# Optimization experiments

Measured on AMD Instinct MI355X. Metric: run time of the kernel, lower is better.

The kernel has to match this reference:

```python
import jax, jax.numpy as jnp
import numpy as np

EPS = 1e-08
K_N = 10
K_E = 10
F_DIM = 512
SCALE = F_DIM ** -0.5
N_NODES = 16384
N_EDGES = 2048


def layernorm(x, w, b):
    mu = x.mean(axis=-1, keepdims=True)
    var = x.var(axis=-1, keepdims=True)
    return (x - mu) * jax.lax.rsqrt(var + 1e-5) * w + b


def mask_attn(attn, k):
    # topk along last dim, scatter boolean mask, elementwise masking
    _, idx = jax.lax.top_k(attn, k)
    rows = jnp.arange(attn.shape[0])[:, None]
    mask = jnp.zeros(attn.shape, dtype=bool).at[rows, idx].set(True)
    return attn * mask


def setup_inputs() -> dict:
    key = jax.random.key(0)
    ks = jax.random.split(key, 12)
    d, h = F_DIM, 512  # hidden = max(f_dim, 128)
    w = 0.02  # weight init scale to keep softmax unsaturated
    return {
        'inputs': jax.random.normal(ks[0], (N_NODES, d), jnp.float32),
        'noise': jax.random.normal(ks[1], (N_EDGES, d), jnp.float32),
        'edges_mu': jax.random.normal(ks[2], (1, d), jnp.float32),
        'edges_logsigma': jnp.zeros((1, d), jnp.float32),
        'Wq': jax.random.normal(ks[3], (d, d), jnp.float32) * w,
        'bq': jnp.zeros((d,), jnp.float32),
        'Wk': jax.random.normal(ks[4], (d, d), jnp.float32) * w,
        'bk': jnp.zeros((d,), jnp.float32),
        'Wv': jax.random.normal(ks[5], (d, d), jnp.float32) * w,
        'bv': jnp.zeros((d,), jnp.float32),
        'W1': jax.random.normal(ks[6], (2 * d, h), jnp.float32) * w,
        'b1': jnp.zeros((h,), jnp.float32),
        'W2': jax.random.normal(ks[7], (h, d), jnp.float32) * w,
        'b2': jnp.zeros((d,), jnp.float32),
        'ln_in_w': jnp.ones((d,), jnp.float32),
        'ln_in_b': jnp.zeros((d,), jnp.float32),
        'ln_e_w': jnp.ones((d,), jnp.float32),
        'ln_e_b': jnp.zeros((d,), jnp.float32),
    }


def reference(inputs, noise, edges_mu, edges_logsigma, Wq, bq, Wk, bk, Wv, bv,
              W1, b1, W2, b2, ln_in_w, ln_in_b, ln_e_w, ln_e_b):
    relu = jax.nn.relu
    # slot init: mu + sigma * noise  -> [n_s, d]
    edges = edges_mu + jnp.exp(edges_logsigma) * noise
    x = layernorm(inputs, ln_in_w, ln_in_b)          # [n, d]
    k = relu(x @ Wk + bk)                            # [n, d]
    v = relu(x @ Wv + bv)                            # [n, d]
    # single iteration (iters=1)
    e = layernorm(edges, ln_e_w, ln_e_b)             # [n_s, d]
    q = relu(e @ Wq + bq)                            # [n_s, d]
    dots = (q @ k.T) * SCALE                         # [n_s, n]
    attn = jax.nn.softmax(dots, axis=1) + EPS
    attn = attn / attn.sum(axis=1, keepdims=True)
    attn = mask_attn(attn, K_N)
    updates = attn @ v                               # [n_s, d]
    e = jnp.concatenate([e, updates], axis=1)        # [n_s, 2d]
    e = relu(e @ W1 + b1) @ W2 + b2                  # mlp -> [n_s, d]
    q2 = x @ Wq + bq                                 # note: no activation here
    k2 = relu(e @ Wk + bk)                           # [n_s, d]
    dots2 = (q2 @ k2.T) * SCALE                      # [n, n_s]
    attn_v = jax.nn.softmax(dots2, axis=1)
    H = mask_attn(attn_v, K_E)
    return e, H, dots2
```

## Files before the change

### kernel.cpp

```cpp
#include <hip/hip_runtime.h>
#include <stdint.h>


#define NN 16384
#define NE 2048
#define TOPK 10

static const float SCALE_F = 0.04419417382415922f;
#define EPS_F 1e-8f

using bf16x8  = __attribute__((ext_vector_type(8))) __bf16;
using floatx4 = __attribute__((ext_vector_type(4))) float;

__device__ __forceinline__ unsigned f_as_u(float f) {
  union { float f; unsigned u; } v; v.f = f; return v.u;
}
__device__ __forceinline__ float u_as_f(unsigned u) {
  union { unsigned u; float f; } v; v.u = u; return v.f;
}
__device__ __forceinline__ unsigned short f2bf(float f) {
  unsigned u = f_as_u(f);
  unsigned r = u + 0x7fffu + ((u >> 16) & 1u);
  return (unsigned short)(r >> 16);
}
__device__ __forceinline__ float bf2f(unsigned short h) {
  return u_as_f(((unsigned)h) << 16);
}

__device__ __forceinline__ void glds16(const unsigned short* g, unsigned short* l) {
  __builtin_amdgcn_global_load_lds(
      (const __attribute__((address_space(1))) unsigned int*)g,
      (__attribute__((address_space(3))) unsigned int*)l, 16, 0, 0);
}

__device__ __forceinline__ unsigned fkey(float f) {
  unsigned u = f_as_u(f);
  return (u & 0x80000000u) ? ~u : (u | 0x80000000u);
}
__device__ __forceinline__ float funkey(unsigned k) {
  unsigned u = (k & 0x80000000u) ? (k ^ 0x80000000u) : ~k;
  return u_as_f(u);
}
__device__ __forceinline__ unsigned long long packkc(float v, int col) {
  return ((unsigned long long)fkey(v) << 32) | (unsigned)(~(unsigned)col);
}
__device__ __forceinline__ int unpack_col(unsigned long long w) {
  return (int)(~(unsigned)(w & 0xFFFFFFFFull));
}
__device__ __forceinline__ float unpack_val(unsigned long long w) {
  return funkey((unsigned)(w >> 32));
}
__device__ __forceinline__ unsigned long long shfl_xor_u64(unsigned long long x, int m) {
  unsigned lo = (unsigned)x, hi = (unsigned)(x >> 32);
  lo = __shfl_xor(lo, m, 64);
  hi = __shfl_xor(hi, m, 64);
  return ((unsigned long long)hi << 32) | lo;
}

__global__ void transpose_all_kernel(
    const float* __restrict__ Wk, const float* __restrict__ Wv,
    const float* __restrict__ Wq, unsigned short* __restrict__ WcatT,
    const float* __restrict__ W1, unsigned short* __restrict__ W1Th,
    unsigned short* __restrict__ W1Tl,
    const float* __restrict__ W2, unsigned short* __restrict__ W2Th,
    unsigned short* __restrict__ W2Tl) {
  __shared__ float tile[32][33];
  int z = blockIdx.z;
  if (z != 3 && blockIdx.y >= 16) return;
  const float* src;
  unsigned short* dhi;
  unsigned short* dlo;
  int K;
  if (z < 3) {
    src = z == 0 ? Wk : (z == 1 ? Wv : Wq);
    dhi = WcatT + (size_t)z * 512 * 512;
    dlo = nullptr; K = 512;
  } else if (z == 3) {
    src = W1; dhi = W1Th; dlo = W1Tl; K = 1024;
  } else {
    src = W2; dhi = W2Th; dlo = W2Tl; K = 512;
  }
  int n0 = blockIdx.x * 32, k0 = blockIdx.y * 32;
  int tx = threadIdx.x, ty = threadIdx.y;
  for (int r = ty; r < 32; r += 8)
    tile[r][tx] = src[(size_t)(k0 + r) * 512 + n0 + tx];
  __syncthreads();
  for (int r = ty; r < 32; r += 8) {
    float v = tile[tx][r];
    size_t o = (size_t)(n0 + r) * K + k0 + tx;
    unsigned short h = f2bf(v);
    dhi[o] = h;
    if (dlo) dlo[o] = f2bf(v - bf2f(h));
  }
}

__device__ __forceinline__ float block_sum_256(float v, float* sm4) {
#pragma unroll
  for (int off = 32; off; off >>= 1) v += __shfl_down(v, off, 64);
  __syncthreads();
  if ((threadIdx.x & 63) == 0) sm4[threadIdx.x >> 6] = v;
  __syncthreads();
  return (sm4[0] + sm4[1]) + (sm4[2] + sm4[3]);
}

__global__ __launch_bounds__(256) void ln_all_kernel(
    const float* __restrict__ in, const float* __restrict__ w,
    const float* __restrict__ b, unsigned short* __restrict__ out_hi,
    const float* __restrict__ noise, const float* __restrict__ mu_e,
    const float* __restrict__ ls_e, const float* __restrict__ we,
    const float* __restrict__ be, unsigned short* __restrict__ e1_hi,
    unsigned short* __restrict__ e1_lo) {
  __shared__ float sm4[4];
  int row = blockIdx.x, tid = threadIdx.x;
  if (row < NN) {
    const float* r = in + (size_t)row * 512;
    float x0 = r[tid], x1 = r[tid + 256];
    float mu = block_sum_256(x0 + x1, sm4) * (1.0f / 512.0f);
    float d0 = x0 - mu, d1 = x1 - mu;
    float var = block_sum_256(d0 * d0 + d1 * d1, sm4) * (1.0f / 512.0f);
    float rs = rsqrtf(var + 1e-5f);
    out_hi[(size_t)row * 512 + tid]       = f2bf(d0 * rs * w[tid] + b[tid]);
    out_hi[(size_t)row * 512 + tid + 256] = f2bf(d1 * rs * w[tid + 256] + b[tid + 256]);
  } else {
    row -= NN;
    const float* r = noise + (size_t)row * 512;
    float x0 = mu_e[tid] + expf(ls_e[tid]) * r[tid];
    float x1 = mu_e[tid + 256] + expf(ls_e[tid + 256]) * r[tid + 256];
    float mu = block_sum_256(x0 + x1, sm4) * (1.0f / 512.0f);
    float d0 = x0 - mu, d1 = x1 - mu;
    float var = block_sum_256(d0 * d0 + d1 * d1, sm4) * (1.0f / 512.0f);
    float rs = rsqrtf(var + 1e-5f);
    float y0 = d0 * rs * we[tid] + be[tid];
    float y1 = d1 * rs * we[tid + 256] + be[tid + 256];
    size_t o = (size_t)row * 1024;
    unsigned short h0 = f2bf(y0), h1 = f2bf(y1);
    e1_hi[o + tid] = h0;             e1_lo[o + tid] = f2bf(y0 - bf2f(h0));
    e1_hi[o + tid + 256] = h1;       e1_lo[o + tid + 256] = f2bf(y1 - bf2f(h1));
  }
}

#define GEMM128_CORE(A_, LDA_, B_, bm_, bn_, acc_, SMEM_)                      \
  unsigned short* As = (unsigned short*)(SMEM_);                               \
  unsigned short* Bs = (unsigned short*)(SMEM_) + 8192;                        \
  {                                                                            \
    int srow = tid >> 3;                                                       \
    int scol = ((tid ^ (tid >> 3)) & 7) << 3;                                  \
    const unsigned short* gA = (A_) + ((bm_) + srow) * (size_t)(LDA_) + scol;  \
    const unsigned short* gB = (B_) + ((bn_) + srow) * (size_t)512 + scol;     \
    unsigned short* dA = As + wave * 512;                                      \
    unsigned short* dB = Bs + wave * 512;                                      \
    int swz0 = (quad ^ (lrow & 7)) << 3;                                       \
    int swz1 = swz0 ^ 32;                                                      \
    int aoff0 = (wave * 32 + lrow) * 64;                                       \
    int aoff1 = aoff0 + 16 * 64;                                               \
    int boffl = lrow * 64;                                                     \
    for (int k0 = 0; k0 < 512; k0 += 64) {                                     \
      glds16(gA + k0, dA);                                                     \
      glds16(gA + 32 * (size_t)(LDA_) + k0, dA + 2048);                        \
      glds16(gA + 64 * (size_t)(LDA_) + k0, dA + 4096);                        \
      glds16(gA + 96 * (size_t)(LDA_) + k0, dA + 6144);                        \
      glds16(gB + k0, dB);                                                     \
      glds16(gB + 32 * 512 + k0, dB + 2048);                                   \
      glds16(gB + 64 * 512 + k0, dB + 4096);                                   \
      glds16(gB + 96 * 512 + k0, dB + 6144);                                   \
      __syncthreads();                                                         \
      bf16x8 af00 = *(const bf16x8*)&As[aoff0 + swz0];                         \
      bf16x8 af01 = *(const bf16x8*)&As[aoff0 + swz1];                         \
      bf16x8 af10 = *(const bf16x8*)&As[aoff1 + swz0];                         \
      bf16x8 af11 = *(const bf16x8*)&As[aoff1 + swz1];                         \
      _Pragma("unroll")                                                        \
      for (int t = 0; t < 8; ++t) {                                            \
        bf16x8 bf0 = *(const bf16x8*)&Bs[t * 1024 + boffl + swz0];             \
        bf16x8 bf1 = *(const bf16x8*)&Bs[t * 1024 + boffl + swz1];             \
        acc_[0][t] = __builtin_amdgcn_mfma_f32_16x16x32_bf16(af00, bf0, acc_[0][t], 0, 0, 0); \
        acc_[0][t] = __builtin_amdgcn_mfma_f32_16x16x32_bf16(af01, bf1, acc_[0][t], 0, 0, 0); \
        acc_[1][t] = __builtin_amdgcn_mfma_f32_16x16x32_bf16(af10, bf0, acc_[1][t], 0, 0, 0); \
        acc_[1][t] = __builtin_amdgcn_mfma_f32_16x16x32_bf16(af11, bf1, acc_[1][t], 0, 0, 0); \
      }                                                                        \
      __syncthreads();                                                         \
    }                                                                          \
  }

#define XCD_PANEL_MAP(mt_, nt_, owns_m_)                                       \
  int xcd = bid & 7, idx = bid >> 3;                                           \
  int per = ((owns_m_) ? (mt_) : (nt_)) >> 3;                                  \
  int pa = idx % per, pb = idx / per;                                          \
  bm = (size_t)((owns_m_) ? (xcd * per + pa) : pb) * 128;                      \
  bn = (size_t)((owns_m_) ? pb : (xcd * per + pa)) * 128;

__global__ __launch_bounds__(256) void gemm128_dots_kernel(
    const unsigned short* __restrict__ A, const unsigned short* __restrict__ B,
    float alpha, float* __restrict__ C, int ldc, int mt, int nt, int owns_m,
    float2* __restrict__ stats) {
  __shared__ __align__(16) char smem[33792];
  int tid = threadIdx.x, wave = tid >> 6, lane = tid & 63;
  int lrow = lane & 15, quad = lane >> 4;
  int bid = (int)blockIdx.x;
  size_t bm, bn;
  XCD_PANEL_MAP(mt, nt, owns_m)
  floatx4 zero4 = {0.f, 0.f, 0.f, 0.f};
  floatx4 acc[2][8];
#pragma unroll
  for (int i = 0; i < 2; ++i)
#pragma unroll
    for (int t = 0; t < 8; ++t) acc[i][t] = zero4;
  GEMM128_CORE(A, 512, B, bm, bn, acc, smem)
  __syncthreads();
  float* wb = (float*)smem + wave * (16 * 132);
#pragma unroll
  for (int i = 0; i < 2; ++i) {
#pragma unroll
    for (int t = 0; t < 8; ++t)
#pragma unroll
      for (int r = 0; r < 4; ++r)
        wb[(quad * 4 + r) * 132 + t * 16 + lrow] = acc[i][t][r] * alpha;
    __syncthreads();
    size_t rowbase = bm + wave * 32 + i * 16;
#pragma unroll
    for (int p = 0; p < 8; ++p) {
      int rr = p * 2 + (lane >> 5);
      float4 v = *(const float4*)&wb[rr * 132 + ((lane & 31) << 2)];
      *(float4*)&C[(rowbase + rr) * (size_t)ldc + bn + ((lane & 31) << 2)] = v;
    }
    __syncthreads();
  }
  if (stats) {
    int j = (int)(bn >> 7);
#pragma unroll
    for (int i = 0; i < 2; ++i) {
#pragma unroll
      for (int r = 0; r < 4; ++r) {
        float mv = acc[i][0][r];
#pragma unroll
        for (int t = 1; t < 8; ++t) mv = fmaxf(mv, acc[i][t][r]);
#pragma unroll
        for (int sft = 1; sft < 16; sft <<= 1)
          mv = fmaxf(mv, __shfl_xor(mv, sft, 64));
        float m = mv * alpha;
        float s = 0.f;
#pragma unroll
        for (int t = 0; t < 8; ++t)
          s += __expf(acc[i][t][r] * alpha - m);
#pragma unroll
        for (int sft = 1; sft < 16; sft <<= 1) s += __shfl_xor(s, sft, 64);
        if (lrow == 0) {
          int row = (int)bm + wave * 32 + i * 16 + quad * 4 + r;
          stats[(size_t)row * 128 + j] = make_float2(m, s);
        }
      }
    }
  }
}

__global__ __launch_bounds__(256) void gemm128_kvq_kernel(
    const unsigned short* __restrict__ X, const unsigned short* __restrict__ E1,
    const unsigned short* __restrict__ B,
    const float* __restrict__ bk, const float* __restrict__ bv,
    const float* __restrict__ bq,
    unsigned short* __restrict__ khi, unsigned short* __restrict__ vhi,
    unsigned short* __restrict__ q2hi, unsigned short* __restrict__ qhi) {
  __shared__ __align__(16) char smem[32768];
  int tid = threadIdx.x, wave = tid >> 6, lane = tid & 63;
  int lrow = lane & 15, quad = lane >> 4;
  int bid = (int)blockIdx.x;
  size_t bm, bn;
  const unsigned short* Aptr;
  int lda;
  unsigned short* dst;
  const float* bias;
  bool relu;
  if (bid < 1536) {
    XCD_PANEL_MAP(128, 12, 1)
    Aptr = X; lda = 512;
    int mat = (int)(bn >> 9);
    bias = mat == 0 ? bk : (mat == 1 ? bv : bq);
    dst = mat == 0 ? khi : (mat == 1 ? vhi : q2hi);
    relu = mat < 2;
  } else {
    int qb = bid - 1536;
    bm = (size_t)(qb >> 2) * 128;
    bn = 1024 + (size_t)(qb & 3) * 128;
    Aptr = E1; lda = 1024;
    dst = qhi; bias = bq; relu = true;
  }
  int colbase = (int)(bn & 511);
  floatx4 zero4 = {0.f, 0.f, 0.f, 0.f};
  floatx4 acc[2][8];
#pragma unroll
  for (int i = 0; i < 2; ++i)
#pragma unroll
    for (int t = 0; t < 8; ++t) acc[i][t] = zero4;
  GEMM128_CORE(Aptr, lda, B, bm, bn, acc, smem)
  __syncthreads();
  unsigned short* wb = (unsigned short*)smem + wave * (16 * 136);
#pragma unroll
  for (int i = 0; i < 2; ++i) {
#pragma unroll
    for (int t = 0; t < 8; ++t) {
      float bvv = bias[colbase + t * 16 + lrow];
#pragma unroll
      for (int r = 0; r < 4; ++r) {
        float v = acc[i][t][r] + bvv;
        if (relu) v = fmaxf(v, 0.0f);
        wb[(quad * 4 + r) * 136 + t * 16 + lrow] = f2bf(v);
      }
    }
    __syncthreads();
    size_t rowbase = bm + wave * 32 + i * 16;
#pragma unroll
    for (int p = 0; p < 4; ++p) {
      int rr = p * 4 + (lane >> 4);
      uint4 v = *(const uint4*)&wb[rr * 136 + ((lane & 15) << 3)];
      *(uint4*)&dst[(rowbase + rr) * 512 + colbase + ((lane & 15) << 3)] = v;
    }
    __syncthreads();
  }
}

template <bool SPLIT, bool RELU, bool HAS_BIAS, bool WF32, bool WHI, bool WLO>
__global__ __launch_bounds__(256) void gemm64_kernel(
    const unsigned short* __restrict__ Ahi, const unsigned short* __restrict__ Alo, int lda,
    const unsigned short* __restrict__ Bhi, const unsigned short* __restrict__ Blo, int K,
    const float* __restrict__ bias, float alpha,
    float* __restrict__ Cf, int ldc,
    unsigned short* __restrict__ Chi, unsigned short* __restrict__ Clo, int ldcb) {
  __shared__ __align__(16) unsigned short AsH[64 * 32];
  __shared__ __align__(16) unsigned short BsH[64 * 32];
  __shared__ __align__(16) unsigned short AsL[64 * 32];
  __shared__ __align__(16) unsigned short BsL[64 * 32];
  int tid = threadIdx.x, wave = tid >> 6, lane = tid & 63;
  int lrow = lane & 15, quad = lane >> 4;
  size_t bm = (size_t)blockIdx.x * 64, bn = (size_t)blockIdx.y * 64;
  int row = tid >> 2, off = (tid & 3) << 3;
  size_t aoff = (bm + row) * (size_t)lda + off;
  size_t boff = (bn + row) * (size_t)K + off;

  floatx4 zero4 = {0.f, 0.f, 0.f, 0.f};
  floatx4 acc[4];
#pragma unroll
  for (int t = 0; t < 4; ++t) acc[t] = zero4;

  uint4 ah = *(const uint4*)(Ahi + aoff);
  uint4 bh = *(const uint4*)(Bhi + boff);
  uint4 al, bl;
  if (SPLIT) {
    al = *(const uint4*)(Alo + aoff);
    bl = *(const uint4*)(Blo + boff);
  }
  for (int k0 = 0; k0 < K; k0 += 32) {
    __syncthreads();
    *(uint4*)&AsH[tid * 8] = ah;
    *(uint4*)&BsH[tid * 8] = bh;
    if (SPLIT) {
      *(uint4*)&AsL[tid * 8] = al;
      *(uint4*)&BsL[tid * 8] = bl;
    }
    __syncthreads();
    if (k0 + 32 < K) {
      ah = *(const uint4*)(Ahi + aoff + k0 + 32);
      bh = *(const uint4*)(Bhi + boff + k0 + 32);
      if (SPLIT) {
        al = *(const uint4*)(Alo + aoff + k0 + 32);
        bl = *(const uint4*)(Blo + boff + k0 + 32);
      }
    }
    int ai = (wave * 16 + lrow) * 32 + quad * 8;
    bf16x8 aH = *(const bf16x8*)&AsH[ai];
    bf16x8 aL;
    if (SPLIT) aL = *(const bf16x8*)&AsL[ai];
#pragma unroll
    for (int t = 0; t < 4; ++t) {
      int bi = (t * 16 + lrow) * 32 + quad * 8;
      bf16x8 bH = *(const bf16x8*)&BsH[bi];
      acc[t] = __builtin_amdgcn_mfma_f32_16x16x32_bf16(aH, bH, acc[t], 0, 0, 0);
      if (SPLIT) {
        bf16x8 bL = *(const bf16x8*)&BsL[bi];
        acc[t] = __builtin_amdgcn_mfma_f32_16x16x32_bf16(aH, bL, acc[t], 0, 0, 0);
        acc[t] = __builtin_amdgcn_mfma_f32_16x16x32_bf16(aL, bH, acc[t], 0, 0, 0);
      }
    }
  }
  size_t row0 = bm + wave * 16 + quad * 4;
#pragma unroll
  for (int t = 0; t < 4; ++t) {
    int col = (int)bn + t * 16 + lrow;
    float bv = HAS_BIAS ? bias[col] : 0.0f;
#pragma unroll
    for (int r = 0; r < 4; ++r) {
      float v = acc[t][r] * alpha + bv;
      if (RELU) v = fmaxf(v, 0.0f);
      if (WF32) Cf[(row0 + r) * (size_t)ldc + col] = v;
      if (WHI) {
        unsigned short h = f2bf(v);
        Chi[(row0 + r) * (size_t)ldcb + col] = h;
        if (WLO) Clo[(row0 + r) * (size_t)ldcb + col] = f2bf(v - bf2f(h));
      }
    }
  }
}

#define INSERT4(lv, li, v, col)                                   \
  do {                                                            \
    if ((v) > lv[3]) {                                            \
      float cv_ = (v); int ci_ = (col);                           \
      _Pragma("unroll")                                           \
      for (int j_ = 0; j_ < 4; ++j_) {                            \
        bool sw_ = (cv_ > lv[j_]);                                \
        float tv_ = sw_ ? lv[j_] : cv_;                           \
        int ti_ = sw_ ? li[j_] : ci_;                              \
        lv[j_] = sw_ ? cv_ : lv[j_];                              \
        li[j_] = sw_ ? ci_ : li[j_];                              \
        cv_ = tv_; ci_ = ti_;                                     \
      }                                                           \
    }                                                             \
  } while (0)

__global__ __launch_bounds__(256) void attn1_kernel(
    const float* __restrict__ dots,
    const float2* __restrict__ stats,
    const unsigned short* __restrict__ vhi,
    unsigned short* __restrict__ e1_hi, unsigned short* __restrict__ e1_lo) {
  __shared__ float sm_m[128], sm_s[128];
  __shared__ unsigned long long sm_key[128];
  __shared__ int clist[128], jpos[128];
  __shared__ int sh_c;
  __shared__ float sh_red[4];
  __shared__ float sh_M, sh_th;
  __shared__ unsigned long long wbest[4];
  __shared__ unsigned long long wkey_s[TOPK];

  int tid = threadIdx.x, wave = tid >> 6, lane = tid & 63;
  int rowi = blockIdx.x;
  const float* drow = dots + (size_t)rowi * NN;

  if (tid < 128) {
    float2 ms = stats[(size_t)rowi * 128 + tid];
    sm_m[tid] = ms.x; sm_s[tid] = ms.y;
    sm_key[tid] = packkc(ms.x, tid);
  }
  if (tid == 0) sh_c = 0;
  __syncthreads();

  if (tid < 128) {
    unsigned long long mykey = sm_key[tid];
    int cnt = 0;
    for (int i = 0; i < 128; ++i) cnt += (sm_key[i] > mykey) ? 1 : 0;
    if (cnt == 0) sh_M = sm_m[tid];
    if (cnt == 9) sh_th = sm_m[tid];
  }
  __syncthreads();
  float M = sh_M, th = sh_th;

  float zp = (tid < 128) ? sm_s[tid] * __expf(sm_m[tid] - M) : 0.f;
#pragma unroll
  for (int off = 32; off; off >>= 1) zp += __shfl_down(zp, off, 64);
  if (lane == 0) sh_red[wave] = zp;
  if (tid < 128 && sm_m[tid] >= th) {
    int p = atomicAdd(&sh_c, 1);
    clist[p] = tid;
    jpos[tid] = p;
  }
  __syncthreads();
  float Z = (sh_red[0] + sh_red[1]) + (sh_red[2] + sh_red[3]);
  int c = sh_c;
  int nel = c << 7;

  float lv[4]; int li[4];
#pragma unroll
  for (int j = 0; j < 4; ++j) { lv[j] = -INFINITY; li[j] = 0x7fffffff; }
  for (int idx = tid; idx < nel; idx += 256) {
    int jj = clist[idx >> 7];
    int col = (jj << 7) + (idx & 127);
    float v = drow[col];
    INSERT4(lv, li, v, col);
  }

  unsigned long long selmask = 0ull;
  int taken = 0;
  for (int rnd = 0; rnd < TOPK; ++rnd) {
    unsigned long long key;
    if (taken < 4) {
      key = packkc(lv[0], li[0]);
    } else {
      key = 0ull;
      int p = 0;
      for (int idx = tid; idx < nel; idx += 256, ++p) {
        if (!((selmask >> p) & 1ull)) {
          int jj = clist[idx >> 7];
          int col = (jj << 7) + (idx & 127);
          unsigned long long kk = packkc(drow[col], col);
          if (kk > key) key = kk;
        }
      }
    }
#pragma unroll
    for (int sft = 32; sft; sft >>= 1) {
      unsigned long long ok = shfl_xor_u64(key, sft);
      if (ok > key) key = ok;
    }
    if (lane == 0) wbest[wave] = key;
    __syncthreads();
    unsigned long long w = wbest[0];
    if (wbest[1] > w) w = wbest[1];
    if (wbest[2] > w) w = wbest[2];
    if (wbest[3] > w) w = wbest[3];
    if (tid == 0) wkey_s[rnd] = w;
    int wcol = unpack_col(w);
    int widx = (jpos[wcol >> 7] << 7) + (wcol & 127);
    if ((widx & 255) == tid) {
      selmask |= (1ull << (widx >> 8));
      if (taken < 4) {
#pragma unroll
        for (int j = 0; j < 3; ++j) { lv[j] = lv[j + 1]; li[j] = li[j + 1]; }
      }
      ++taken;
    }
    __syncthreads();
  }

  const float inv_den = 1.0f / (1.0f + (float)NN * EPS_F);
  float invZ = 1.0f / Z;
  float u0 = 0.f, u1 = 0.f;
#pragma unroll
  for (int j = 0; j < TOPK; ++j) {
    unsigned long long w = wkey_s[j];
    int col = unpack_col(w);
    float val = unpack_val(w);
    float a = (__expf(val - M) * invZ + EPS_F) * inv_den;
    const unsigned short* vr = vhi + (size_t)col * 512;
    u0 += a * bf2f(vr[tid]);
    u1 += a * bf2f(vr[tid + 256]);
  }
  size_t o = (size_t)rowi * 1024 + 512;
  unsigned short h0 = f2bf(u0), h1 = f2bf(u1);
  e1_hi[o + tid] = h0;             e1_lo[o + tid] = f2bf(u0 - bf2f(h0));
  e1_hi[o + tid + 256] = h1;       e1_lo[o + tid + 256] = f2bf(u1 - bf2f(h1));
}

__global__ __launch_bounds__(256) void attn2_kernel(const float* __restrict__ dots2,
                                                    float* __restrict__ Hout) {
  int tid = threadIdx.x, wave = tid >> 6, lane = tid & 63;
  int rowi = blockIdx.x * 4 + wave;
  const float4* r4 = (const float4*)(dots2 + (size_t)rowi * NE);

  float d[32];
  float m = -INFINITY;
#pragma unroll
  for (int i = 0; i < 8; ++i) {
    float4 q = r4[lane + (i << 6)];
#pragma unroll
    for (int c = 0; c < 4; ++c) {
      d[i * 4 + c] = (&q.x)[c];
      m = fmaxf(m, d[i * 4 + c]);
    }
  }
#pragma unroll
  for (int sft = 32; sft; sft >>= 1) m = fmaxf(m, __shfl_xor(m, sft, 64));

  float s = 0.f;
#pragma unroll
  for (int j = 0; j < 32; ++j) { d[j] = __expf(d[j] - m); s += d[j]; }
#pragma unroll
  for (int sft = 32; sft; sft >>= 1) s += __shfl_xor(s, sft, 64);
  float invZ = 1.0f / s;

  float lv[4]; int li[4];
#pragma unroll
  for (int j = 0; j < 4; ++j) { lv[j] = -INFINITY; li[j] = 0x7fffffff; }
#pragma unroll
  for (int i = 0; i < 8; ++i) {
#pragma unroll
    for (int c = 0; c < 4; ++c) {
      int col = ((lane + (i << 6)) << 2) + c;
      INSERT4(lv, li, d[i * 4 + c], col);
    }
  }

  unsigned selmask = 0;
  int taken = 0;
  for (int rnd = 0; rnd < TOPK; ++rnd) {
    unsigned long long key;
    if (taken < 4) {
      key = packkc(lv[0], li[0]);
    } else {
      key = 0ull;
#pragma unroll
      for (int j = 0; j < 32; ++j) {
        if (!((selmask >> j) & 1u)) {
          int col = ((lane + ((j >> 2) << 6)) << 2) + (j & 3);
          unsigned long long kk = packkc(d[j], col);
          if (kk > key) key = kk;
        }
      }
    }
#pragma unroll
    for (int sft = 32; sft; sft >>= 1) {
      unsigned long long ok = shfl_xor_u64(key, sft);
      if (ok > key) key = ok;
    }
    int wcol = unpack_col(key);
    if (((wcol >> 2) & 63) == lane) {
      int sl = ((wcol >> 8) << 2) | (wcol & 3);
      selmask |= (1u << sl);
      if (taken < 4) {
#pragma unroll
        for (int j = 0; j < 3; ++j) { lv[j] = lv[j + 1]; li[j] = li[j + 1]; }
      }
      ++taken;
    }
  }

  float* hr = Hout + (size_t)rowi * NE;
#pragma unroll
  for (int i = 0; i < 8; ++i) {
    float4 o;
#pragma unroll
    for (int c = 0; c < 4; ++c) {
      int sl = i * 4 + c;
      (&o.x)[c] = ((selmask >> sl) & 1u) ? d[sl] * invZ : 0.0f;
    }
    ((float4*)hr)[lane + (i << 6)] = o;
  }
}

extern "C" void kernel_launch(void* const* d_in, const int* in_sizes, int n_in,
                              void* d_out, int out_size, void* d_ws, size_t ws_size,
                              hipStream_t stream) {
  (void)in_sizes; (void)n_in; (void)out_size; (void)ws_size;
  const float* inputs  = (const float*)d_in[0];
  const float* noise   = (const float*)d_in[1];
  const float* edges_mu = (const float*)d_in[2];
  const float* edges_ls = (const float*)d_in[3];
  const float* Wq = (const float*)d_in[4];
  const float* bq = (const float*)d_in[5];
  const float* Wk = (const float*)d_in[6];
  const float* bk = (const float*)d_in[7];
  const float* Wv = (const float*)d_in[8];
  const float* bv = (const float*)d_in[9];
  const float* W1 = (const float*)d_in[10];
  const float* b1 = (const float*)d_in[11];
  const float* W2 = (const float*)d_in[12];
  const float* b2 = (const float*)d_in[13];
  const float* ln_in_w = (const float*)d_in[14];
  const float* ln_in_b = (const float*)d_in[15];
  const float* ln_e_w = (const float*)d_in[16];
  const float* ln_e_b = (const float*)d_in[17];

  float* out_e  = (float*)d_out;
  float* out_H  = out_e + (size_t)NE * 512;
  float* out_d2 = out_H + (size_t)NN * NE;

  const size_t MB = 1024 * 1024;
  unsigned char* hb = (unsigned char*)out_H;
  unsigned short* x_hi  = (unsigned short*)(hb);
  unsigned short* k_hi  = (unsigned short*)(hb + 16 * MB);
  unsigned short* v_hi  = (unsigned short*)(hb + 32 * MB);
  unsigned short* q2_hi = (unsigned short*)(hb + 48 * MB);
  unsigned short* WcatT = (unsigned short*)(hb + 64 * MB);
  unsigned short* W1Th  = (unsigned short*)(hb + 66 * MB);
  unsigned short* W1Tl  = (unsigned short*)(hb + 67 * MB);
  unsigned short* W2Th  = (unsigned short*)(hb + 68 * MB);
  unsigned short* W2Tl  = (unsigned short*)(hb + 68 * MB + 512 * 1024);
  unsigned short* e1_hi = (unsigned short*)(hb + 70 * MB);
  unsigned short* e1_lo = (unsigned short*)(hb + 74 * MB);
  unsigned short* q_hi  = (unsigned short*)(hb + 78 * MB);
  unsigned short* h_hi  = (unsigned short*)(hb + 80 * MB);
  unsigned short* h_lo  = (unsigned short*)(hb + 82 * MB);
  unsigned short* e_hi  = (unsigned short*)(hb + 84 * MB);
  float2* stats1        = (float2*)(hb + 86 * MB);
  unsigned short* WkT   = WcatT;
  float* dots = out_d2;
  unsigned short* k2_hi = (unsigned short*)d_ws;

  dim3 tb(256);
  dim3 t32(32, 8);

  transpose_all_kernel<<<dim3(16, 32, 5), t32, 0, stream>>>(
      Wk, Wv, Wq, WcatT, W1, W1Th, W1Tl, W2, W2Th, W2Tl);
  ln_all_kernel<<<NN + NE, tb, 0, stream>>>(
      inputs, ln_in_w, ln_in_b, x_hi,
      noise, edges_mu, edges_ls, ln_e_w, ln_e_b, e1_hi, e1_lo);

  gemm128_kvq_kernel<<<dim3(1600), tb, 0, stream>>>(
      x_hi, e1_hi, WcatT, bk, bv, bq, k_hi, v_hi, q2_hi, q_hi);
  gemm128_dots_kernel<<<dim3(2048), tb, 0, stream>>>(
      q_hi, k_hi, SCALE_F, dots, NN, 16, 128, 0, stats1);
  attn1_kernel<<<NE, tb, 0, stream>>>(dots, stats1, v_hi, e1_hi, e1_lo);
  gemm64_kernel<true, true, true, false, true, true><<<dim3(32, 8), tb, 0, stream>>>(
      e1_hi, e1_lo, 1024, W1Th, W1Tl, 1024, b1, 1.f, nullptr, 0, h_hi, h_lo, 512);
  gemm64_kernel<true, false, true, true, true, false><<<dim3(32, 8), tb, 0, stream>>>(
      h_hi, h_lo, 512, W2Th, W2Tl, 512, b2, 1.f, out_e, 512, e_hi, nullptr, 512);
  gemm64_kernel<false, true, true, false, true, false><<<dim3(32, 8), tb, 0, stream>>>(
      e_hi, nullptr, 512, WkT, nullptr, 512, bk, 1.f, nullptr, 0, k2_hi, nullptr, 512);
  gemm128_dots_kernel<<<dim3(2048), tb, 0, stream>>>(
      q2_hi, k2_hi, SCALE_F, out_d2, NE, 128, 16, 1, nullptr);
  attn2_kernel<<<NN / 4, tb, 0, stream>>>(out_d2, out_H);
}
```

Baseline: 551.6 us.

## Replace 128x128 dots GEMM with 256x256 tile, 8-wave pipelined MFMA kernel

Both dots GEMMs (q·kᵀ and q2·k2ᵀ) now use a 256x256 tile kernel with 512 threads. It stages tiles through a 128KB LDS ring via direct global-to-LDS loads, using explicit vmcnt waits, barriers and setprio around MFMA phases. The softmax row statistics move from register shuffles into the LDS epilogue. The larger tile is meant to raise arithmetic intensity and overlap loads with MFMA, at the cost of heavy LDS use, lower occupancy and a hand-scheduled pipeline that is fragile.

```diff
diff --git a/kernel.cpp b/kernel.cpp
--- a/kernel.cpp
+++ b/kernel.cpp
@@ -188,67 +188,162 @@
   bm = (size_t)((owns_m_) ? (xcd * per + pa) : pb) * 128;                      \
   bn = (size_t)((owns_m_) ? pb : (xcd * per + pa)) * 128;
 
-__global__ __launch_bounds__(256) void gemm128_dots_kernel(
+
+#define NOVM ((void)0)
+#define VM2 asm volatile("s_waitcnt vmcnt(2)" ::: "memory")
+#define VM0 asm volatile("s_waitcnt vmcnt(0)" ::: "memory")
+#define NOSTAGE ((void)0)
+
+#define STAGE(G_, rowbase_, kb_, slotptr_)                                     \
+  { const unsigned short* g0_ =                                                \
+        (G_) + ((rowbase_) + (size_t)sr0) * 512 + (kb_) + sc0;                 \
+    const unsigned short* g1_ =                                                \
+        (G_) + ((rowbase_) + (size_t)sr1) * 512 + (kb_) + sc1;                 \
+    glds16(g0_, (unsigned short*)((char*)(slotptr_) + wave * 1024));           \
+    glds16(g1_, (unsigned short*)((char*)(slotptr_) + 8192 + wave * 1024)); }
+
+#define PHASE(IM0_, IN0_, ASL_, BSL_, STAGE_STMT_, VM_)                        \
+  {                                                                            \
+    const char* Ap_ = ldsA_c + (ASL_) * 16384;                                 \
+    const char* Bp_ = ldsB_c + (BSL_) * 16384;                                 \
+    bf16x8 af_[4][2], bg_[2][2];                                               \
+    _Pragma("unroll") for (int i_ = 0; i_ < 4; ++i_) {                         \
+      af_[i_][0] = *(const bf16x8*)(Ap_ + aoff0 + i_ * 4096);                  \
+      af_[i_][1] = *(const bf16x8*)(Ap_ + aoff1 + i_ * 4096);                  \
+    }                                                                          \
+    _Pragma("unroll") for (int j_ = 0; j_ < 2; ++j_) {                         \
+      bg_[j_][0] = *(const bf16x8*)(Bp_ + boff0 + j_ * 8192);                  \
+      bg_[j_][1] = *(const bf16x8*)(Bp_ + boff1 + j_ * 8192);                  \
+    }                                                                          \
+    STAGE_STMT_;                                                               \
+    VM_;                                                                       \
+    __builtin_amdgcn_sched_barrier(0);                                         \
+    __builtin_amdgcn_s_barrier();                                              \
+    __builtin_amdgcn_sched_barrier(0);                                         \
+    __builtin_amdgcn_s_setprio(1);                                             \
+    _Pragma("unroll") for (int i_ = 0; i_ < 4; ++i_)                           \
+      _Pragma("unroll") for (int j_ = 0; j_ < 2; ++j_) {                       \
+        acc[(IM0_) + i_][(IN0_) + j_] =                                        \
+            __builtin_amdgcn_mfma_f32_16x16x32_bf16(                           \
+                af_[i_][0], bg_[j_][0], acc[(IM0_) + i_][(IN0_) + j_], 0, 0, 0);\
+        acc[(IM0_) + i_][(IN0_) + j_] =                                        \
+            __builtin_amdgcn_mfma_f32_16x16x32_bf16(                           \
+                af_[i_][1], bg_[j_][1], acc[(IM0_) + i_][(IN0_) + j_], 0, 0, 0);\
+      }                                                                        \
+    __builtin_amdgcn_s_setprio(0);                                             \
+  }
+
+#define GEMM256_CORE(A_, B_)                                                   \
+  __shared__ __align__(16) char lds_all[131072];                               \
+  char* ldsA_s = lds_all;                                                      \
+  char* ldsB_s = lds_all + 65536;                                              \
+  const char* ldsA_c = lds_all;                                                \
+  const char* ldsB_c = lds_all + 65536;                                        \
+  int tid = threadIdx.x, wave = tid >> 6, lane = tid & 63;                     \
+  int lrow = lane & 15, quad = lane >> 4;                                      \
+  int wfm = wave >> 2, wfn = wave & 3;                                         \
+  int smask = ((lrow >> 2) & 3) << 5;                                          \
+  int aoff0 = (wfm * 16 + lrow) * 128 + ((quad * 16) ^ smask);                 \
+  int aoff1 = aoff0 ^ 64;                                                      \
+  int boff0 = (wfn * 16 + lrow) * 128 + ((quad * 16) ^ smask);                 \
+  int boff1 = boff0 ^ 64;                                                      \
+  int p0_ = tid * 16, l0_ = p0_ ^ (((p0_ >> 9) & 3) << 5);                     \
+  int sr0 = l0_ >> 7, sc0 = (l0_ & 127) >> 1;                                  \
+  int p1_ = 8192 + tid * 16, l1_ = p1_ ^ (((p1_ >> 9) & 3) << 5);              \
+  int sr1 = l1_ >> 7, sc1 = (l1_ & 127) >> 1;                                  \
+  floatx4 acc[8][4];                                                           \
+  { floatx4 z4_ = {0.f, 0.f, 0.f, 0.f};                                        \
+    _Pragma("unroll") for (int i_ = 0; i_ < 8; ++i_)                           \
+      _Pragma("unroll") for (int j_ = 0; j_ < 4; ++j_) acc[i_][j_] = z4_; }    \
+        \
+  STAGE(A_, bm, 0, ldsA_s)                                                     \
+  STAGE(B_, bn, 0, ldsB_s)                                                     \
+  STAGE(A_, bm + 128, 0, ldsA_s + 16384)                                       \
+  STAGE(B_, bn + 128, 0, ldsB_s + 16384)                                       \
+  STAGE(A_, bm, 64, ldsA_s + 32768)                                            \
+  VM2;                                                                         \
+  __builtin_amdgcn_sched_barrier(0);                                           \
+  __builtin_amdgcn_s_barrier();                                                \
+  __builtin_amdgcn_sched_barrier(0);                                           \
+  for (int t2 = 0; t2 < 8; t2 += 2) {                                          \
+    int kn = (t2 + 1) * 64, kn2 = (t2 + 2) * 64, kn3 = (t2 + 3) * 64;          \
+    PHASE(0, 0, 0, 0, STAGE(B_, bn, kn, ldsB_s + 32768), NOVM)                 \
+    PHASE(0, 2, 0, 1, STAGE(A_, bm + 128, kn, ldsA_s + 49152), NOVM)           \
+    PHASE(4, 0, 1, 0, STAGE(B_, bn + 128, kn, ldsB_s + 49152), NOVM)           \
+    if (t2 < 6) {                                                              \
+      PHASE(4, 2, 1, 1, STAGE(A_, bm, kn2, ldsA_s), VM2)                       \
+      PHASE(0, 0, 2, 2, STAGE(B_, bn, kn2, ldsB_s), NOVM)                      \
+      PHASE(0, 2, 2, 3, STAGE(A_, bm + 128, kn2, ldsA_s + 16384), NOVM)        \
+      PHASE(4, 0, 3, 2, STAGE(B_, bn + 128, kn2, ldsB_s + 16384), NOVM)        \
+      PHASE(4, 2, 3, 3, STAGE(A_, bm, kn3, ldsA_s + 32768), VM2)               \
+    } else {                                                                   \
+      PHASE(4, 2, 1, 1, NOSTAGE, VM0)                                          \
+      PHASE(0, 0, 2, 2, NOSTAGE, NOVM)                                         \
+      PHASE(0, 2, 2, 3, NOSTAGE, NOVM)                                         \
+      PHASE(4, 0, 3, 2, NOSTAGE, NOVM)                                         \
+      PHASE(4, 2, 3, 3, NOSTAGE, NOVM)                                         \
+    }                                                                          \
+    (void)kn3;                                                                 \
+  }
+
+__global__ __launch_bounds__(512, 2) void gemm256_dots_kernel(
     const unsigned short* __restrict__ A, const unsigned short* __restrict__ B,
     float alpha, float* __restrict__ C, int ldc, int mt, int nt, int owns_m,
     float2* __restrict__ stats) {
-  __shared__ __align__(16) char smem[33792];
-  int tid = threadIdx.x, wave = tid >> 6, lane = tid & 63;
-  int lrow = lane & 15, quad = lane >> 4;
   int bid = (int)blockIdx.x;
   size_t bm, bn;
-  XCD_PANEL_MAP(mt, nt, owns_m)
-  floatx4 zero4 = {0.f, 0.f, 0.f, 0.f};
-  floatx4 acc[2][8];
-#pragma unroll
-  for (int i = 0; i < 2; ++i)
-#pragma unroll
-    for (int t = 0; t < 8; ++t) acc[i][t] = zero4;
-  GEMM128_CORE(A, 512, B, bm, bn, acc, smem)
+  {
+    int xcd = bid & 7, idx = bid >> 3;
+    int per = (owns_m ? mt : nt) >> 3;
+    int pa = idx % per, pb = idx / per;
+    bm = (size_t)(owns_m ? (xcd * per + pa) : pb) * 256;
+    bn = (size_t)(owns_m ? pb : (xcd * per + pa)) * 256;
+  }
+  GEMM256_CORE(A, B)
   __syncthreads();
-  float* wb = (float*)smem + wave * (16 * 132);
-#pragma unroll
-  for (int i = 0; i < 2; ++i) {
-#pragma unroll
-    for (int t = 0; t < 8; ++t)
-#pragma unroll
-      for (int r = 0; r < 4; ++r)
-        wb[(quad * 4 + r) * 132 + t * 16 + lrow] = acc[i][t][r] * alpha;
+  float* eb = (float*)lds_all;
+#pragma unroll
+  for (int g = 0; g < 4; ++g) {
+#pragma unroll
+    for (int imh = 0; imh < 2; ++imh) {
+      int im = 2 * g + imh;
+      int rloc = imh * 32 + wfm * 16 + quad * 4;
+#pragma unroll
+      for (int in = 0; in < 4; ++in) {
+        int cloc = in * 64 + wfn * 16 + lrow;
+#pragma unroll
+        for (int r = 0; r < 4; ++r)
+          eb[(rloc + r) * 260 + cloc] = acc[im][in][r] * alpha;
+      }
+    }
     __syncthreads();
-    size_t rowbase = bm + wave * 32 + i * 16;
+    size_t rowg = bm + 64 * g;
 #pragma unroll
     for (int p = 0; p < 8; ++p) {
-      int rr = p * 2 + (lane >> 5);
-      float4 v = *(const float4*)&wb[rr * 132 + ((lane & 31) << 2)];
-      *(float4*)&C[(rowbase + rr) * (size_t)ldc + bn + ((lane & 31) << 2)] = v;
+      int f = tid + (p << 9);
+      int rr = f >> 6, c4 = (f & 63) << 2;
+      float4 v = *(const float4*)&eb[rr * 260 + c4];
+      *(float4*)&C[(rowg + rr) * (size_t)ldc + bn + c4] = v;
+    }
+    if (stats) {
+      int task = tid >> 2, sub = tid & 3;
+      int rr = task >> 1, jt = task & 1;
+      const float* base = &eb[rr * 260 + jt * 128 + sub * 32];
+      float mv = base[0];
+#pragma unroll
+      for (int u = 1; u < 32; ++u) mv = fmaxf(mv, base[u]);
+#pragma unroll
+      for (int sft = 1; sft < 4; sft <<= 1)
+        mv = fmaxf(mv, __shfl_xor(mv, sft, 64));
+      float sl = 0.f;
+#pragma unroll
+      for (int u = 0; u < 32; ++u) sl += __expf(base[u] - mv);
+#pragma unroll
+      for (int sft = 1; sft < 4; sft <<= 1) sl += __shfl_xor(sl, sft, 64);
+      if (sub == 0)
+        stats[(rowg + rr) * 128 + (int)(bn >> 7) + jt] = make_float2(mv, sl);
     }
     __syncthreads();
-  }
-  if (stats) {
-    int j = (int)(bn >> 7);
-#pragma unroll
-    for (int i = 0; i < 2; ++i) {
-#pragma unroll
-      for (int r = 0; r < 4; ++r) {
-        float mv = acc[i][0][r];
-#pragma unroll
-        for (int t = 1; t < 8; ++t) mv = fmaxf(mv, acc[i][t][r]);
-#pragma unroll
-        for (int sft = 1; sft < 16; sft <<= 1)
-          mv = fmaxf(mv, __shfl_xor(mv, sft, 64));
-        float m = mv * alpha;
-        float s = 0.f;
-#pragma unroll
-        for (int t = 0; t < 8; ++t)
-          s += __expf(acc[i][t][r] * alpha - m);
-#pragma unroll
-        for (int sft = 1; sft < 16; sft <<= 1) s += __shfl_xor(s, sft, 64);
-        if (lrow == 0) {
-          int row = (int)bm + wave * 32 + i * 16 + quad * 4 + r;
-          stats[(size_t)row * 128 + j] = make_float2(m, s);
-        }
-      }
-    }
   }
 }
 
@@ -683,8 +778,8 @@
 
   gemm128_kvq_kernel<<<dim3(1600), tb, 0, stream>>>(
       x_hi, e1_hi, WcatT, bk, bv, bq, k_hi, v_hi, q2_hi, q_hi);
-  gemm128_dots_kernel<<<dim3(2048), tb, 0, stream>>>(
-      q_hi, k_hi, SCALE_F, dots, NN, 16, 128, 0, stats1);
+  gemm256_dots_kernel<<<dim3(512), dim3(512), 0, stream>>>(
+      q_hi, k_hi, SCALE_F, dots, NN, 8, 64, 0, stats1);
   attn1_kernel<<<NE, tb, 0, stream>>>(dots, stats1, v_hi, e1_hi, e1_lo);
   gemm64_kernel<true, true, true, false, true, true><<<dim3(32, 8), tb, 0, stream>>>(
       e1_hi, e1_lo, 1024, W1Th, W1Tl, 1024, b1, 1.f, nullptr, 0, h_hi, h_lo, 512);
@@ -692,7 +787,7 @@
       h_hi, h_lo, 512, W2Th, W2Tl, 512, b2, 1.f, out_e, 512, e_hi, nullptr, 512);
   gemm64_kernel<false, true, true, false, true, false><<<dim3(32, 8), tb, 0, stream>>>(
       e_hi, nullptr, 512, WkT, nullptr, 512, bk, 1.f, nullptr, 0, k2_hi, nullptr, 512);
-  gemm128_dots_kernel<<<dim3(2048), tb, 0, stream>>>(
-      q2_hi, k2_hi, SCALE_F, out_d2, NE, 128, 16, 1, nullptr);
+  gemm256_dots_kernel<<<dim3(512), dim3(512), 0, stream>>>(
+      q2_hi, k2_hi, SCALE_F, out_d2, NE, 64, 8, 1, nullptr);
   attn2_kernel<<<NN / 4, tb, 0, stream>>>(out_d2, out_H);
 }
```

New measurement: 777.8 us. +41.0%, slower.
